# Kernel optimization log

Measured on AMD Instinct MI355X. Metric: run time of the kernel, lower is better.

## Reference

```python
import jax, jax.numpy as jnp
import numpy as np

NUM_ATTRS = 8    # A: number of attribute names in attr_map
NUM_VALS = 16    # V: number of distinct values per attribute


def setup_inputs() -> dict:
    key = jax.random.key(0)
    k1, k2 = jax.random.split(key)
    B, D = 2_000_000, 8
    predictions = jax.random.normal(k1, (B, D), dtype=jnp.float32)
    attr_vals = jax.random.randint(k2, (B, NUM_ATTRS), 0, NUM_VALS, dtype=jnp.int32)
    return {"predictions": predictions, "attr_vals": attr_vals}


def reference(predictions, attr_vals):
    B, A = attr_vals.shape
    V = NUM_VALS
    # per-node mean of sigmoid probs; stacking rows then .mean() == mean of per-node means
    per_node = jnp.mean(jax.nn.sigmoid(predictions), axis=1)  # [B]
    # flatten (attr, value) groups into A*V segments
    seg_ids = (attr_vals + jnp.arange(A, dtype=attr_vals.dtype)[None, :] * V).reshape(-1)  # [B*A]
    vals = jnp.broadcast_to(per_node[:, None], (B, A)).reshape(-1)  # [B*A]
    sums = jax.ops.segment_sum(vals, seg_ids, num_segments=A * V)
    counts = jax.ops.segment_sum(jnp.ones_like(vals), seg_ids, num_segments=A * V)
    means = (sums / jnp.maximum(counts, 1.0)).reshape(A, V)      # [A, V]
    present = (counts > 0).reshape(A, V)                          # [A, V]
    # pairwise squared diffs of group means within each attribute (i < j)
    diff = means[:, :, None] - means[:, None, :]                  # [A, V, V]
    triu = jnp.triu(jnp.ones((V, V), dtype=bool), k=1)
    pair_mask = present[:, :, None] & present[:, None, :] & triu[None, :, :]
    total_loss = jnp.sum(jnp.where(pair_mask, diff * diff, 0.0))
    num_comparisons = jnp.sum(pair_mask)
    return jnp.where(num_comparisons > 0, total_loss / num_comparisons, 0.0)
```

## Files before the change

kernel.cpp:

```cpp
#include <hip/hip_runtime.h>

#define NA 8
#define NV 16
#define NS (NA * NV)
#define NW 4
#define NR 2
#define FIX_SHIFT 43
#define FIX_MASK ((1ULL << FIX_SHIFT) - 1)
#define FIX_SCALE_D 16384.0
#define CNT_SH 23
#define CELL_MASK ((1u << CNT_SH) - 1)


__device__ __forceinline__ float sig(float x) {
    return __builtin_amdgcn_rcpf(1.0f + __expf(-x));
}

__device__ __forceinline__ void process_chunk(
    float4 p, int4 a, int lane, unsigned int* __restrict__ hw)
{
    float hs = sig(p.x) + sig(p.y) + sig(p.z) + sig(p.w);
    float s  = hs + __shfl_xor(hs, 1, 64);
    unsigned int fixed = (unsigned int)(s * 2048.0f);
    unsigned int add   = (1u << CNT_SH) | fixed;
    const int abase = (lane & 1) << 2;
    atomicAdd(&hw[((abase + 0) << 4) + a.x], add);
    atomicAdd(&hw[((abase + 1) << 4) + a.y], add);
    atomicAdd(&hw[((abase + 2) << 4) + a.z], add);
    atomicAdd(&hw[((abase + 3) << 4) + a.w], add);
}

__global__ __launch_bounds__(256) void k1_accum(
    const float* __restrict__ preds,
    const int*   __restrict__ attrs,
    unsigned long long* __restrict__ partials,
    int* __restrict__ counter,
    int B, int nb)
{
    __shared__ unsigned int h[NW][NR][NS];
    for (int i = threadIdx.x; i < NW * NR * NS; i += 256)
        ((unsigned int*)h)[i] = 0u;
    if (blockIdx.x == 0 && threadIdx.x == 0)
        __hip_atomic_store(counter, 0, __ATOMIC_RELAXED,
                           __HIP_MEMORY_SCOPE_AGENT);
    __syncthreads();

    const int lane = threadIdx.x & 63;
    const int wave = threadIdx.x >> 6;
    unsigned int* __restrict__ hw = h[wave][lane >> 5];

    const float4* __restrict__ p4 = (const float4*)preds;
    const int4*   __restrict__ a4 = (const int4*)attrs;

    const int gw      = blockIdx.x * NW + wave;
    const int nwv     = nb * NW;
    const int nchunks = B >> 5;

    int c = gw;
    if (c < nchunks) {
        float4 p = p4[(size_t)c * 64 + lane];
        int4   a = a4[(size_t)c * 64 + lane];
        for (;;) {
            const int  cn   = c + nwv;
            const bool more = (cn < nchunks);
            float4 pn; int4 an;
            if (more) {
                pn = p4[(size_t)cn * 64 + lane];
                an = a4[(size_t)cn * 64 + lane];
            }
            process_chunk(p, a, lane, hw);
            if (!more) break;
            p = pn; a = an; c = cn;
        }
    }

    const int rem = B & 31;
    if (rem && blockIdx.x == 0 && wave == 0 && lane < rem * 2) {
        const size_t base = (size_t)(B >> 5) * 64;
        float4 p = p4[base + lane];
        int4   a = a4[base + lane];
        process_chunk(p, a, lane, hw);
    }
    __syncthreads();

    if (threadIdx.x < NS) {
        unsigned long long cnt = 0ULL, fix = 0ULL;
        #pragma unroll
        for (int w = 0; w < NW; ++w)
            #pragma unroll
            for (int r = 0; r < NR; ++r) {
                unsigned int cell = h[w][r][threadIdx.x];
                cnt += (cell >> CNT_SH);
                fix += (cell & CELL_MASK);
            }
        partials[(size_t)threadIdx.x * nb + blockIdx.x] =
            (cnt << FIX_SHIFT) | fix;
    }
}

__global__ __launch_bounds__(256) void k2_reduce_finalize(
    const unsigned long long* __restrict__ partials,
    double* __restrict__ means,
    int*    __restrict__ pres,
    int*    __restrict__ counter,
    float*  __restrict__ out,
    int nb)
{
    const int s = blockIdx.x;
    unsigned long long sum = 0ULL;
    unsigned int cnt = 0u;
    for (int b = threadIdx.x; b < nb; b += 256) {
        unsigned long long p = partials[(size_t)s * nb + b];
        cnt += (unsigned int)(p >> FIX_SHIFT);
        sum += (p & FIX_MASK);
    }
    for (int off = 32; off > 0; off >>= 1) {
        sum += __shfl_down(sum, off, 64);
        cnt += __shfl_down(cnt, off, 64);
    }
    __shared__ unsigned long long ws_[4];
    __shared__ unsigned int wc_[4];
    const int wave = threadIdx.x >> 6;
    if ((threadIdx.x & 63) == 0) { ws_[wave] = sum; wc_[wave] = cnt; }
    __syncthreads();

    __shared__ int lastFlag;
    if (threadIdx.x == 0) {
        unsigned long long S = ws_[0] + ws_[1] + ws_[2] + ws_[3];
        unsigned int C = wc_[0] + wc_[1] + wc_[2] + wc_[3];
        double m = C ? ((double)S * (1.0 / FIX_SCALE_D)) / (double)C : 0.0;
        __hip_atomic_store(&means[s], m, __ATOMIC_RELEASE,
                           __HIP_MEMORY_SCOPE_AGENT);
        __hip_atomic_store(&pres[s], C ? 1 : 0, __ATOMIC_RELEASE,
                           __HIP_MEMORY_SCOPE_AGENT);
        int old = __hip_atomic_fetch_add(counter, 1, __ATOMIC_ACQ_REL,
                                         __HIP_MEMORY_SCOPE_AGENT);
        lastFlag = (old == NS - 1);
    }
    __syncthreads();
    if (!lastFlag) return;

    __shared__ double s_mean[NS];
    __shared__ int    s_pres[NS];
    const int t = threadIdx.x;
    if (t < NS) {
        s_mean[t] = __hip_atomic_load(&means[t], __ATOMIC_ACQUIRE,
                                      __HIP_MEMORY_SCOPE_AGENT);
        s_pres[t] = __hip_atomic_load(&pres[t], __ATOMIC_ACQUIRE,
                                      __HIP_MEMORY_SCOPE_AGENT);
    }
    __syncthreads();

    double loss = 0.0;
    int    ncmp = 0;
    if (t < NS && s_pres[t]) {
        const int a = t >> 4;
        const int i = t & (NV - 1);
        const double mi = s_mean[t];
        for (int j = i + 1; j < NV; ++j) {
            const int sj = a * NV + j;
            if (s_pres[sj]) {
                const double d = mi - s_mean[sj];
                loss += d * d;
                ncmp += 1;
            }
        }
    }
    for (int off = 32; off > 0; off >>= 1) {
        loss += __shfl_down(loss, off, 64);
        ncmp += __shfl_down(ncmp, off, 64);
    }
    __shared__ double w_loss[4];
    __shared__ int    w_ncmp[4];
    if ((t & 63) == 0) { w_loss[wave] = loss; w_ncmp[wave] = ncmp; }
    __syncthreads();
    if (t == 0) {
        const double total = w_loss[0] + w_loss[1] + w_loss[2] + w_loss[3];
        const int    n     = w_ncmp[0] + w_ncmp[1] + w_ncmp[2] + w_ncmp[3];
        out[0] = (n > 0) ? (float)(total / (double)n) : 0.0f;
    }
}

extern "C" void kernel_launch(void* const* d_in, const int* in_sizes, int n_in,
                              void* d_out, int out_size, void* d_ws, size_t ws_size,
                              hipStream_t stream) {
    const float* preds = (const float*)d_in[0];
    const int*   attrs = (const int*)d_in[1];
    float*       out   = (float*)d_out;

    const int B = in_sizes[1] / NA;

    const size_t tail = NS * sizeof(double) + NS * sizeof(int) + sizeof(int);
    int nb = 2048;
    if (ws_size < (size_t)NS * nb * sizeof(unsigned long long) + tail) nb = 1024;

    unsigned long long* partials = (unsigned long long*)d_ws;
    double* means = (double*)((char*)d_ws +
                              (size_t)NS * nb * sizeof(unsigned long long));
    int*    pres    = (int*)(means + NS);
    int*    counter = pres + NS;

    k1_accum<<<nb, 256, 0, stream>>>(preds, attrs, partials, counter, B, nb);
    k2_reduce_finalize<<<NS, 256, 0, stream>>>(partials, means, pres,
                                               counter, out, nb);
}
```

Baseline: 156.3 us.

## Split fused sigmoid-histogram kernel into separate sigmoid and histogram passes

```diff
diff --git a/kernel.cpp b/kernel.cpp
--- a/kernel.cpp
+++ b/kernel.cpp
@@ -16,41 +16,71 @@
     return __builtin_amdgcn_rcpf(1.0f + __expf(-x));
 }
 
-__device__ __forceinline__ void process_chunk(
-    float4 p, int4 a, int lane, unsigned int* __restrict__ hw)
+__global__ __launch_bounds__(256) void k1a_sigmoid(
+    const float* __restrict__ preds,
+    float* __restrict__ per_node,
+    int* __restrict__ counter,
+    int B, int nb)
 {
-    float hs = sig(p.x) + sig(p.y) + sig(p.z) + sig(p.w);
-    float s  = hs + __shfl_xor(hs, 1, 64);
-    unsigned int fixed = (unsigned int)(s * 2048.0f);
-    unsigned int add   = (1u << CNT_SH) | fixed;
-    const int abase = (lane & 1) << 2;
-    atomicAdd(&hw[((abase + 0) << 4) + a.x], add);
-    atomicAdd(&hw[((abase + 1) << 4) + a.y], add);
-    atomicAdd(&hw[((abase + 2) << 4) + a.z], add);
-    atomicAdd(&hw[((abase + 3) << 4) + a.w], add);
-}
-
-__global__ __launch_bounds__(256) void k1_accum(
-    const float* __restrict__ preds,
+    if (blockIdx.x == 0 && threadIdx.x == 0)
+        __hip_atomic_store(counter, 0, __ATOMIC_RELAXED,
+                           __HIP_MEMORY_SCOPE_AGENT);
+
+    const int lane = threadIdx.x & 63;
+    const int wave = threadIdx.x >> 6;
+    const int gw   = blockIdx.x * NW + wave;
+    const int nwv  = nb * NW;
+    const int nchunks = B >> 5;
+
+    const float4* __restrict__ p4 = (const float4*)preds;
+
+    int c = gw;
+    if (c < nchunks) {
+        float4 p = p4[(size_t)c * 64 + lane];
+        for (;;) {
+            const int  cn   = c + nwv;
+            const bool more = (cn < nchunks);
+            float4 pn;
+            if (more) pn = p4[(size_t)cn * 64 + lane];
+            {
+                float hs = sig(p.x) + sig(p.y) + sig(p.z) + sig(p.w);
+                float s  = hs + __shfl_xor(hs, 1, 64);
+                if (!(lane & 1))
+                    per_node[c * 32 + (lane >> 1)] = s * 0.125f;
+            }
+            if (!more) break;
+            p = pn; c = cn;
+        }
+    }
+
+    const int rem = B & 31;
+    if (rem && blockIdx.x == 0 && wave == 0 && lane < rem * 2) {
+        const int rbase = B & ~31;
+        float4 p = p4[(size_t)(B >> 5) * 64 + lane];
+        float hs = sig(p.x) + sig(p.y) + sig(p.z) + sig(p.w);
+        float s  = hs + __shfl_xor(hs, 1, 64);
+        if (!(lane & 1))
+            per_node[rbase + (lane >> 1)] = s * 0.125f;
+    }
+}
+
+__global__ __launch_bounds__(256) void k1b_hist(
+    const float* __restrict__ per_node,
     const int*   __restrict__ attrs,
     unsigned long long* __restrict__ partials,
-    int* __restrict__ counter,
     int B, int nb)
 {
     __shared__ unsigned int h[NW][NR][NS];
     for (int i = threadIdx.x; i < NW * NR * NS; i += 256)
         ((unsigned int*)h)[i] = 0u;
-    if (blockIdx.x == 0 && threadIdx.x == 0)
-        __hip_atomic_store(counter, 0, __ATOMIC_RELAXED,
-                           __HIP_MEMORY_SCOPE_AGENT);
     __syncthreads();
 
     const int lane = threadIdx.x & 63;
     const int wave = threadIdx.x >> 6;
     unsigned int* __restrict__ hw = h[wave][lane >> 5];
-
-    const float4* __restrict__ p4 = (const float4*)preds;
-    const int4*   __restrict__ a4 = (const int4*)attrs;
+    const int abase = (lane & 1) << 2;
+
+    const int4* __restrict__ a4 = (const int4*)attrs;
 
     const int gw      = blockIdx.x * NW + wave;
     const int nwv     = nb * NW;
@@ -58,28 +88,39 @@
 
     int c = gw;
     if (c < nchunks) {
-        float4 p = p4[(size_t)c * 64 + lane];
-        int4   a = a4[(size_t)c * 64 + lane];
+        int4  a = a4[(size_t)c * 64 + lane];
+        float v = per_node[c * 32 + (lane >> 1)];
         for (;;) {
             const int  cn   = c + nwv;
             const bool more = (cn < nchunks);
-            float4 pn; int4 an;
+            int4 an; float vn;
             if (more) {
-                pn = p4[(size_t)cn * 64 + lane];
                 an = a4[(size_t)cn * 64 + lane];
-            }
-            process_chunk(p, a, lane, hw);
+                vn = per_node[cn * 32 + (lane >> 1)];
+            }
+            {
+                unsigned int add = (1u << CNT_SH)
+                                 | (unsigned int)(v * 16384.0f);
+                atomicAdd(&hw[((abase + 0) << 4) + a.x], add);
+                atomicAdd(&hw[((abase + 1) << 4) + a.y], add);
+                atomicAdd(&hw[((abase + 2) << 4) + a.z], add);
+                atomicAdd(&hw[((abase + 3) << 4) + a.w], add);
+            }
             if (!more) break;
-            p = pn; a = an; c = cn;
+            a = an; v = vn; c = cn;
         }
     }
 
     const int rem = B & 31;
     if (rem && blockIdx.x == 0 && wave == 0 && lane < rem * 2) {
-        const size_t base = (size_t)(B >> 5) * 64;
-        float4 p = p4[base + lane];
-        int4   a = a4[base + lane];
-        process_chunk(p, a, lane, hw);
+        const int rbase = B & ~31;
+        int4  a = a4[(size_t)(B >> 5) * 64 + lane];
+        float v = per_node[rbase + (lane >> 1)];
+        unsigned int add = (1u << CNT_SH) | (unsigned int)(v * 16384.0f);
+        atomicAdd(&hw[((abase + 0) << 4) + a.x], add);
+        atomicAdd(&hw[((abase + 1) << 4) + a.y], add);
+        atomicAdd(&hw[((abase + 2) << 4) + a.z], add);
+        atomicAdd(&hw[((abase + 3) << 4) + a.w], add);
     }
     __syncthreads();
 
@@ -190,17 +231,20 @@
 
     const int B = in_sizes[1] / NA;
 
-    const size_t tail = NS * sizeof(double) + NS * sizeof(int) + sizeof(int);
+    const size_t tail = (size_t)B * sizeof(float)
+                      + NS * sizeof(double) + NS * sizeof(int) + sizeof(int);
     int nb = 2048;
     if (ws_size < (size_t)NS * nb * sizeof(unsigned long long) + tail) nb = 1024;
 
     unsigned long long* partials = (unsigned long long*)d_ws;
-    double* means = (double*)((char*)d_ws +
-                              (size_t)NS * nb * sizeof(unsigned long long));
-    int*    pres    = (int*)(means + NS);
-    int*    counter = pres + NS;
-
-    k1_accum<<<nb, 256, 0, stream>>>(preds, attrs, partials, counter, B, nb);
+    float*  per_node = (float*)((char*)d_ws +
+                                (size_t)NS * nb * sizeof(unsigned long long));
+    double* means    = (double*)(per_node + B);
+    int*    pres     = (int*)(means + NS);
+    int*    counter  = pres + NS;
+
+    k1a_sigmoid<<<nb, 256, 0, stream>>>(preds, per_node, counter, B, nb);
+    k1b_hist<<<nb, 256, 0, stream>>>(per_node, attrs, partials, B, nb);
     k2_reduce_finalize<<<NS, 256, 0, stream>>>(partials, means, pres,
                                                counter, out, nb);
 }
```

Result: no change. 154.3 us (-1.3%).

## Stream inputs into LDS with a 4-deep async global_load_lds pipeline

Applied to the files above, without the earlier changes.

```diff
diff --git a/kernel.cpp b/kernel.cpp
--- a/kernel.cpp
+++ b/kernel.cpp
@@ -5,6 +5,7 @@
 #define NS (NA * NV)
 #define NW 4
 #define NR 2
+#define DEPTH 4
 #define FIX_SHIFT 43
 #define FIX_MASK ((1ULL << FIX_SHIFT) - 1)
 #define FIX_SCALE_D 16384.0
@@ -12,18 +13,19 @@
 #define CELL_MASK ((1u << CNT_SH) - 1)
 
 
+typedef const __attribute__((address_space(1))) void* gas_vp;
+typedef __attribute__((address_space(3))) void* las_vp;
+
 __device__ __forceinline__ float sig(float x) {
     return __builtin_amdgcn_rcpf(1.0f + __expf(-x));
 }
 
-__device__ __forceinline__ void process_chunk(
-    float4 p, int4 a, int lane, unsigned int* __restrict__ hw)
+__device__ __forceinline__ void hist_update(
+    float4 p, int4 a, int abase, unsigned int* __restrict__ hw)
 {
     float hs = sig(p.x) + sig(p.y) + sig(p.z) + sig(p.w);
     float s  = hs + __shfl_xor(hs, 1, 64);
-    unsigned int fixed = (unsigned int)(s * 2048.0f);
-    unsigned int add   = (1u << CNT_SH) | fixed;
-    const int abase = (lane & 1) << 2;
+    unsigned int add = (1u << CNT_SH) | (unsigned int)(s * 2048.0f);
     atomicAdd(&hw[((abase + 0) << 4) + a.x], add);
     atomicAdd(&hw[((abase + 1) << 4) + a.y], add);
     atomicAdd(&hw[((abase + 2) << 4) + a.z], add);
@@ -38,6 +40,9 @@
     int B, int nb)
 {
     __shared__ unsigned int h[NW][NR][NS];
+    __shared__ float4 sp[NW][DEPTH][64];
+    __shared__ int4   sa[NW][DEPTH][64];
+
     for (int i = threadIdx.x; i < NW * NR * NS; i += 256)
         ((unsigned int*)h)[i] = 0u;
     if (blockIdx.x == 0 && threadIdx.x == 0)
@@ -48,6 +53,7 @@
     const int lane = threadIdx.x & 63;
     const int wave = threadIdx.x >> 6;
     unsigned int* __restrict__ hw = h[wave][lane >> 5];
+    const int abase = (lane & 1) << 2;
 
     const float4* __restrict__ p4 = (const float4*)preds;
     const int4*   __restrict__ a4 = (const int4*)attrs;
@@ -56,30 +62,74 @@
     const int nwv     = nb * NW;
     const int nchunks = B >> 5;
 
+    #define STAGE(slot, cc)                                                   \
+    {                                                                         \
+        __builtin_amdgcn_global_load_lds(                                     \
+            (gas_vp)(p4 + (size_t)(cc) * 64 + lane),                          \
+            (las_vp)&sp[wave][slot][0], 16, 0, 0);                            \
+        __builtin_amdgcn_global_load_lds(                                     \
+            (gas_vp)(a4 + (size_t)(cc) * 64 + lane),                          \
+            (las_vp)&sa[wave][slot][0], 16, 0, 0);                            \
+    }
+
     int c = gw;
     if (c < nchunks) {
-        float4 p = p4[(size_t)c * 64 + lane];
-        int4   a = a4[(size_t)c * 64 + lane];
+        {
+            int c1 = (c + 1 * nwv < nchunks) ? c + 1 * nwv : c;
+            int c2 = (c + 2 * nwv < nchunks) ? c + 2 * nwv : c;
+            int c3 = (c + 3 * nwv < nchunks) ? c + 3 * nwv : c;
+            STAGE(0, c); STAGE(1, c1); STAGE(2, c2); STAGE(3, c3);
+        }
         for (;;) {
-            const int  cn   = c + nwv;
-            const bool more = (cn < nchunks);
-            float4 pn; int4 an;
-            if (more) {
-                pn = p4[(size_t)cn * 64 + lane];
-                an = a4[(size_t)cn * 64 + lane];
-            }
-            process_chunk(p, a, lane, hw);
-            if (!more) break;
-            p = pn; a = an; c = cn;
+            asm volatile("s_waitcnt vmcnt(6)" ::: "memory");
+            {
+                float4 p = sp[wave][0][lane];
+                int4   a = sa[wave][0][lane];
+                hist_update(p, a, abase, hw);
+                asm volatile("" ::: "memory");
+                int cn = c + 4 * nwv;
+                STAGE(0, (cn < nchunks) ? cn : c);
+            }
+            c += nwv; if (c >= nchunks) break;
+            asm volatile("s_waitcnt vmcnt(6)" ::: "memory");
+            {
+                float4 p = sp[wave][1][lane];
+                int4   a = sa[wave][1][lane];
+                hist_update(p, a, abase, hw);
+                asm volatile("" ::: "memory");
+                int cn = c + 4 * nwv;
+                STAGE(1, (cn < nchunks) ? cn : c);
+            }
+            c += nwv; if (c >= nchunks) break;
+            asm volatile("s_waitcnt vmcnt(6)" ::: "memory");
+            {
+                float4 p = sp[wave][2][lane];
+                int4   a = sa[wave][2][lane];
+                hist_update(p, a, abase, hw);
+                asm volatile("" ::: "memory");
+                int cn = c + 4 * nwv;
+                STAGE(2, (cn < nchunks) ? cn : c);
+            }
+            c += nwv; if (c >= nchunks) break;
+            asm volatile("s_waitcnt vmcnt(6)" ::: "memory");
+            {
+                float4 p = sp[wave][3][lane];
+                int4   a = sa[wave][3][lane];
+                hist_update(p, a, abase, hw);
+                asm volatile("" ::: "memory");
+                int cn = c + 4 * nwv;
+                STAGE(3, (cn < nchunks) ? cn : c);
+            }
+            c += nwv; if (c >= nchunks) break;
         }
     }
+    #undef STAGE
 
     const int rem = B & 31;
     if (rem && blockIdx.x == 0 && wave == 0 && lane < rem * 2) {
-        const size_t base = (size_t)(B >> 5) * 64;
-        float4 p = p4[base + lane];
-        int4   a = a4[base + lane];
-        process_chunk(p, a, lane, hw);
+        float4 p = p4[(size_t)(B >> 5) * 64 + lane];
+        int4   a = a4[(size_t)(B >> 5) * 64 + lane];
+        hist_update(p, a, abase, hw);
     }
     __syncthreads();
 
@@ -190,13 +240,11 @@
 
     const int B = in_sizes[1] / NA;
 
-    const size_t tail = NS * sizeof(double) + NS * sizeof(int) + sizeof(int);
-    int nb = 2048;
-    if (ws_size < (size_t)NS * nb * sizeof(unsigned long long) + tail) nb = 1024;
+    const int nb = 1024;
 
     unsigned long long* partials = (unsigned long long*)d_ws;
-    double* means = (double*)((char*)d_ws +
-                              (size_t)NS * nb * sizeof(unsigned long long));
+    double* means   = (double*)((char*)d_ws +
+                                (size_t)NS * nb * sizeof(unsigned long long));
     int*    pres    = (int*)(means + NS);
     int*    counter = pres + NS;
 
```

New measurement: 152.3 us. -2.6%, faster.
